# Kernel tuning notes

Measured on AMD Instinct MI355X. Metric: run time of the kernel, lower is better.

Reference implementation:

```python
import jax, jax.numpy as jnp
import numpy as np

N, E, D, ED = 10000, 50000, 32, 16
DIMS = [(D, 8 * D), (8 * D, 16 * D), (16 * D, 16 * D), (16 * D, 16 * D)]
BI_OUT = 8 * D + ED  # 272


def _gat(h, src, dst, ea, Wl, Wr, We, att, b, n):
    """GATv2Conv, heads=1: score = att . leaky_relu(Wl x_j + Wr x_i + We e_ij); msg = Wl x_j."""
    xl = h @ Wl
    xr = h @ Wr
    ee = ea @ We
    s = jax.nn.leaky_relu(xl[src] + xr[dst] + ee, 0.2)   # [E_aug, out]
    alpha = s @ att                                       # [E_aug]
    amax = jax.lax.stop_gradient(jax.ops.segment_max(alpha, dst, num_segments=n))
    ex = jnp.exp(alpha - amax[dst])
    den = jax.ops.segment_sum(ex, dst, num_segments=n)
    w = ex / jnp.maximum(den[dst], 1e-16)
    return jax.ops.segment_sum(xl[src] * w[:, None], dst, num_segments=n) + b


def _forward(x, edge_attr, Wl0, Wr0, We0, a0, b0, Wl1, Wr1, We1, a1, b1,
             Wl2, Wr2, We2, a2, b2, Wl3, Wr3, We3, a3, b3,
             Wbi, bbi, Wm1, bm1, Wm2, bm2, Wm3, bm3, edge_index):
    src, dst = edge_index[0], edge_index[1]
    # self loops with edge_attr fill_value='mean' (mean of incoming edge_attr per target node)
    cnt = jax.ops.segment_sum(jnp.ones((E,), jnp.float32), dst, num_segments=N)
    mean_attr = jax.ops.segment_sum(edge_attr, dst, num_segments=N) / jnp.maximum(cnt, 1.0)[:, None]
    loop = jnp.arange(N, dtype=edge_index.dtype)
    src_a = jnp.concatenate([src, loop])
    dst_a = jnp.concatenate([dst, loop])
    ea_a = jnp.concatenate([edge_attr, mean_attr], axis=0)

    h = x
    layers = [(Wl0, Wr0, We0, a0, b0), (Wl1, Wr1, We1, a1, b1),
              (Wl2, Wr2, We2, a2, b2), (Wl3, Wr3, We3, a3, b3)]
    for i, (Wl, Wr, We, a, b) in enumerate(layers):
        h = _gat(h, src_a, dst_a, ea_a, Wl, Wr, We, a, b, N)
        if i < 3:
            h = jax.nn.relu(h)

    # edge scoring: gather both endpoints, bilinear with edge_attr, then MLP -> sigmoid
    z = jnp.concatenate([h[src], h[dst]], axis=1)           # [E, 2*16*D] = [E, 1024]
    bi = jnp.einsum('ni,kij,nj->nk', z, Wbi, edge_attr) + bbi  # [E, 272]
    m = jax.nn.relu(bi @ Wm1 + bm1)
    m = jax.nn.relu(m @ Wm2 + bm2)
    return jax.nn.sigmoid(m @ Wm3 + bm3)                    # [E, 1]


def setup_inputs() -> dict:
    ki = iter(jax.random.split(jax.random.key(0), 40))

    def rn(shape, s=0.05):
        return jax.random.normal(next(ki), shape, dtype=jnp.float32) * s

    inp = {
        "x": rn((N, D), 1.0),
        "edge_attr": rn((E, ED), 1.0),
        "edge_index": jax.random.randint(next(ki), (2, E), 0, N, dtype=jnp.int32),
    }
    for i, (din, dout) in enumerate(DIMS):
        inp[f"Wl{i}"] = rn((din, dout))
        inp[f"Wr{i}"] = rn((din, dout))
        inp[f"We{i}"] = rn((ED, dout))
        inp[f"a{i}"] = rn((dout,))
        inp[f"b{i}"] = jnp.zeros((dout,), jnp.float32)
    inp["Wbi"] = rn((BI_OUT, 2 * 16 * D, ED), 0.02)
    inp["bbi"] = jnp.zeros((BI_OUT,), jnp.float32)
    inp["Wm1"] = rn((BI_OUT, BI_OUT))
    inp["bm1"] = jnp.zeros((BI_OUT,), jnp.float32)
    inp["Wm2"] = rn((BI_OUT, D))
    inp["bm2"] = jnp.zeros((D,), jnp.float32)
    inp["Wm3"] = rn((D, 1))
    inp["bm3"] = jnp.zeros((1,), jnp.float32)
    return inp


def reference(x, edge_attr, edge_index, Wl0, Wr0, We0, a0, b0, Wl1, Wr1, We1, a1, b1,
              Wl2, Wr2, We2, a2, b2, Wl3, Wr3, We3, a3, b3,
              Wbi, bbi, Wm1, bm1, Wm2, bm2, Wm3, bm3):
    return _forward(x, edge_attr, Wl0, Wr0, We0, a0, b0, Wl1, Wr1, We1, a1, b1,
                    Wl2, Wr2, We2, a2, b2, Wl3, Wr3, We3, a3, b3,
                    Wbi, bbi, Wm1, bm1, Wm2, bm2, Wm3, bm3, edge_index)
```

## Files before the change

### kernel.cpp

```cpp
#include <hip/hip_runtime.h>
#include <hip/hip_bf16.h>
#include <hip/hip_fp16.h>
#include <cstdio>

#define N_NODES 10000
#define M_NODEP 10240
#define N_EDGES 50000
#define M_EDGEP 50176
#define E_AUG   60000
#define E_AUGP  60160
#define ED      16
#define BI_OUT  272
#define KP      288

typedef __attribute__((ext_vector_type(8))) short s16x8;
typedef __attribute__((ext_vector_type(4))) short s16x4;
typedef __attribute__((ext_vector_type(8))) _Float16 h16x8;
typedef __attribute__((ext_vector_type(4))) _Float16 h16x4;
typedef __attribute__((ext_vector_type(4))) float f32x4;

__device__ inline void stc(float* p, float v){ *p = v; }
__device__ inline void stc(__hip_bfloat16* p, float v){ *p = __float2bfloat16(v); }
__device__ inline void stc(__half* p, float v){ *p = __float2half(v); }
__device__ inline float bf2f(short s){ return __uint_as_float(((unsigned)(unsigned short)s) << 16); }
__device__ inline short f2bf(float f){ __hip_bfloat16 h = __float2bfloat16(f); return *(short*)&h; }

__device__ __forceinline__ void gl2lds16(const void* g, void* l){
  __builtin_amdgcn_global_load_lds((const __attribute__((address_space(1))) void*)g,
                                   (__attribute__((address_space(3))) void*)l, 16, 0, 0);
}

__device__ inline size_t preidx(int n, int k, int kSteps){
  int nb = n >> 7, f = (n >> 4) & 7, r = n & 15;
  int s = k >> 5, q = (k >> 3) & 3, ii = k & 7;
  return ((((size_t)nb*kSteps + s)*8 + f)*64 + q*16 + r)*8 + ii;
}

__global__ void edge_attr_sum_k(const float* __restrict__ ea, const int* __restrict__ ei,
                                float* __restrict__ meanat, float* __restrict__ cntF){
  int t = blockIdx.x*256 + threadIdx.x;
  if (t >= N_EDGES*ED) return;
  int e = t >> 4, j = t & 15;
  int dst = ei[N_EDGES + e];
  atomicAdd(&meanat[dst*ED + j], ea[t]);
  if (j == 0) atomicAdd(&cntF[dst], 1.0f);
}

__global__ void mean_div_k(float* __restrict__ meanat, const float* __restrict__ cntF){
  int t = blockIdx.x*256 + threadIdx.x;
  if (t >= N_NODES*ED) return;
  meanat[t] /= fmaxf(cntF[t>>4], 1.0f);
}

__global__ void scan_k(const float* __restrict__ cntF, int* __restrict__ rowptr){
  __shared__ int s[1024];
  int tid = threadIdx.x;
  int loc[10]; int sum = 0;
  #pragma unroll
  for (int k = 0; k < 10; ++k){
    int i = tid*10 + k;
    int v = (i < N_NODES) ? ((int)cntF[i] + 1) : 0;
    loc[k] = sum; sum += v;
  }
  s[tid] = sum; __syncthreads();
  for (int off = 1; off < 1024; off <<= 1){
    int t2 = (tid >= off) ? s[tid-off] : 0;
    __syncthreads();
    s[tid] += t2;
    __syncthreads();
  }
  int pre = s[tid] - sum;
  #pragma unroll
  for (int k = 0; k < 10; ++k){
    int i = tid*10 + k;
    if (i < N_NODES) rowptr[i] = pre + loc[k];
  }
  if (tid == 1023) rowptr[N_NODES] = s[1023];
}

__global__ void scatter_k(const int* __restrict__ ei, const int* __restrict__ rowptr,
                          int* __restrict__ fill, int* __restrict__ csr){
  int e = blockIdx.x*256 + threadIdx.x;
  if (e >= E_AUG) return;
  int dst = (e < N_EDGES) ? ei[N_EDGES+e] : (e - N_EDGES);
  int pos = rowptr[dst] + atomicAdd(&fill[dst], 1);
  csr[pos] = e;
}

template<typename TC, bool BIAS, bool RELU>
__global__ __launch_bounds__(256)
void mfma_gemm_k(const __hip_bfloat16* __restrict__ A, const __hip_bfloat16* __restrict__ Bp,
                 TC* __restrict__ C, const float* __restrict__ bias,
                 int Mstore, int K, int lda, int ldc){
  __shared__ __align__(16) __hip_bfloat16 Asm[2][4096];
  const int tid = threadIdx.x;
  const int lane = tid & 63, wave = tid >> 6;
  const int wm = (wave >> 1) * 64, wn = (wave & 1) * 64;
  const int m0 = blockIdx.x * 128, n0 = blockIdx.y * 128;
  const int quad = lane >> 4, r16 = lane & 15;
  const int kSteps = K >> 5;

  f32x4 acc[4][4];
  #pragma unroll
  for (int i = 0; i < 4; ++i)
    #pragma unroll
    for (int j = 0; j < 4; ++j)
      acc[i][j] = (f32x4){0.f, 0.f, 0.f, 0.f};

  const int rl = lane >> 2, cq = lane & 3;
  const int row0 = wave*32 + rl;
  const int qg = (cq - ((row0 >> 1) & 3)) & 3;
  const __hip_bfloat16* ga0 = &A[(size_t)(m0 + row0)*lda + qg*8];
  const __hip_bfloat16* ga1 = &A[(size_t)(m0 + row0 + 16)*lda + qg*8];
  const int aoff0 = (wave*32)*32, aoff1 = (wave*32 + 16)*32;

  const __hip_bfloat16* gB = Bp + (((size_t)blockIdx.y*kSteps)*8 + (wn >> 4))*512 + (size_t)lane*8;

  gl2lds16(ga0, &Asm[0][aoff0]);
  gl2lds16(ga1, &Asm[0][aoff1]);
  s16x8 bcur[4], bnxt[4];
  #pragma unroll
  for (int j = 0; j < 4; ++j) bcur[j] = *(const s16x8*)(gB + j*512);

  for (int s = 0; s < kSteps; ++s){
    __syncthreads();
    if (s + 1 < kSteps){
      int k0 = (s + 1) * 32;
      gl2lds16(ga0 + k0, &Asm[(s+1)&1][aoff0]);
      gl2lds16(ga1 + k0, &Asm[(s+1)&1][aoff1]);
      const __hip_bfloat16* gBn = gB + (size_t)(s+1)*4096;
      #pragma unroll
      for (int j = 0; j < 4; ++j) bnxt[j] = *(const s16x8*)(gBn + j*512);
    }
    s16x8 af[4];
    #pragma unroll
    for (int i = 0; i < 4; ++i){
      int row = wm + i*16 + r16;
      af[i] = *(const s16x8*)&Asm[s & 1][row*32 + (((quad + (row >> 1)) & 3) << 3)];
    }
    #pragma unroll
    for (int i = 0; i < 4; ++i)
      #pragma unroll
      for (int j = 0; j < 4; ++j)
        acc[i][j] = __builtin_amdgcn_mfma_f32_16x16x32_bf16(af[i], bcur[j], acc[i][j], 0, 0, 0);
    #pragma unroll
    for (int j = 0; j < 4; ++j) bcur[j] = bnxt[j];
  }
  #pragma unroll
  for (int i = 0; i < 4; ++i){
    #pragma unroll
    for (int reg = 0; reg < 4; ++reg){
      int gr = m0 + wm + i*16 + quad*4 + reg;
      if (gr >= Mstore) continue;
      #pragma unroll
      for (int j = 0; j < 4; ++j){
        int gc = n0 + wn + j*16 + r16;
        float v = acc[i][j][reg];
        if (BIAS) v += bias[gc];
        if (RELU) v = fmaxf(v, 0.f);
        stc(&C[(size_t)gr*ldc + gc], v);
      }
    }
  }
}

__global__ void prep_weights_k(
    const float* __restrict__ Wl0, const float* __restrict__ Wr0, const float* __restrict__ We0,
    const float* __restrict__ Wl1, const float* __restrict__ Wr1, const float* __restrict__ We1,
    const float* __restrict__ Wl2, const float* __restrict__ Wr2, const float* __restrict__ We2,
    const float* __restrict__ Wl3, const float* __restrict__ Wr3, const float* __restrict__ We3,
    const float* __restrict__ Wm1, const float* __restrict__ bm1,
    const float* __restrict__ Wm2, const float* __restrict__ bm2,
    __hip_bfloat16* __restrict__ WTa, __hip_bfloat16* __restrict__ WeTa,
    __hip_bfloat16* __restrict__ Wm1T, __hip_bfloat16* __restrict__ Wm2T,
    float* __restrict__ bm1p, float* __restrict__ bm2p){
  int t = blockIdx.x*256 + threadIdx.x;
  if (t < 16384){
    int half = t >> 13, r = t & 8191, i = r >> 8, j = r & 255;
    WTa[preidx(half*256 + j, i, 1)] = __float2bfloat16(half ? Wr0[r] : Wl0[r]);
  } else if (t < 278528){
    int u = t - 16384, half = u >> 17, r = u & 131071, i = r >> 9, j = r & 511;
    WTa[16384 + preidx(half*512 + j, i, 8)] = __float2bfloat16(half ? Wr1[r] : Wl1[r]);
  } else if (t < 802816){
    int u = t - 278528, half = u >> 18, r = u & 262143, i = r >> 9, j = r & 511;
    WTa[278528 + preidx(half*512 + j, i, 16)] = __float2bfloat16(half ? Wr2[r] : Wl2[r]);
  } else if (t < 1327104){
    int u = t - 802816, half = u >> 18, r = u & 262143, i = r >> 9, j = r & 511;
    WTa[802816 + preidx(half*512 + j, i, 16)] = __float2bfloat16(half ? Wr3[r] : Wl3[r]);
  }
  if (t < 8192){
    int n = t >> 5, k = t & 31;
    WeTa[preidx(n, k, 1)] = __float2bfloat16((k < 16) ? We0[k*256 + n] : 0.f);
  } else if (t < 24576){
    int u = t - 8192, n = u >> 5, k = u & 31;
    WeTa[8192 + preidx(n, k, 1)] = __float2bfloat16((k < 16) ? We1[k*512 + n] : 0.f);
  } else if (t < 40960){
    int u = t - 24576, n = u >> 5, k = u & 31;
    WeTa[24576 + preidx(n, k, 1)] = __float2bfloat16((k < 16) ? We2[k*512 + n] : 0.f);
  } else if (t < 57344){
    int u = t - 40960, n = u >> 5, k = u & 31;
    WeTa[40960 + preidx(n, k, 1)] = __float2bfloat16((k < 16) ? We3[k*512 + n] : 0.f);
  }
  if (t < 384*KP){
    int n = t / KP, k = t - n*KP;
    Wm1T[preidx(n, k, 9)] = __float2bfloat16((n < BI_OUT && k < BI_OUT) ? Wm1[(size_t)k*BI_OUT + n] : 0.f);
  }
  if (t < 128*KP){
    int n = t / KP, k = t - n*KP;
    Wm2T[preidx(n, k, 9)] = __float2bfloat16((n < 32 && k < BI_OUT) ? Wm2[(size_t)k*32 + n] : 0.f);
  }
  if (t < 384) bm1p[t] = (t < BI_OUT) ? bm1[t] : 0.f;
  if (t < 128) bm2p[t] = (t < 32) ? bm2[t] : 0.f;
}

__global__ void cast_h_k(const float* __restrict__ h, __hip_bfloat16* __restrict__ hb, int K){
  int t = blockIdx.x*256 + threadIdx.x;
  if (t >= M_NODEP*K) return;
  int r = t / K;
  hb[t] = (r < N_NODES) ? __float2bfloat16(h[t]) : __float2bfloat16(0.f);
}

__global__ void cast_ea_k(const float* __restrict__ ea, const float* __restrict__ meanat,
                          __hip_bfloat16* __restrict__ eab){
  int t = blockIdx.x*256 + threadIdx.x;
  if (t >= E_AUGP*32) return;
  int e = t >> 5, j = t & 31;
  float v = 0.f;
  if (j < 16){
    if (e < N_EDGES) v = ea[(size_t)e*ED + j];
    else if (e < E_AUG) v = meanat[(size_t)(e - N_EDGES)*ED + j];
  }
  eab[t] = __float2bfloat16(v);
}

__global__ void wbi_transpose_k(const float* __restrict__ Wbi, __hip_bfloat16* __restrict__ WtAll){
  int t = blockIdx.x*256 + threadIdx.x;
  if (t >= BI_OUT*1024*ED) return;
  int k = t >> 14, r = t & 16383;
  int i = r >> 4, j = r & 15;
  int c = (k < 136) ? 0 : 1;
  int kb = c*136;
  const int cw = 2176;
  size_t baseE = (size_t)c * 2228224;
  int row = ((i >= 512) ? cw : 0) + (k - kb)*16 + j;
  WtAll[baseE + preidx(row, i & 511, 16)] = __float2bfloat16(Wbi[t]);
}

template<int DOUT, bool RELU>
__global__ __launch_bounds__(256)
void gat_fused_k(const __hip_bfloat16* __restrict__ XLXR, const __half* __restrict__ EE,
                 const int* __restrict__ ei, const int* __restrict__ rowptr,
                 const int* __restrict__ csr, const float* __restrict__ att,
                 const float* __restrict__ b, __hip_bfloat16* __restrict__ hb){
  constexpr int NI = DOUT/64;
  constexpr int W2 = 2*DOUT;
  int wave = threadIdx.x >> 6, lane = threadIdx.x & 63;
  int n = blockIdx.x*4 + wave;
  if (n >= N_NODES) return;
  int r0 = rowptr[n], r1 = rowptr[n+1];
  int pp = r0 + lane;
  int e_l = 0, s_l = 0;
  if (pp < r1){
    e_l = csr[pp];
    s_l = (e_l < N_EDGES) ? ei[e_l] : (e_l - N_EDGES);
  }
  float xr[NI], at[NI], acc[NI];
  #pragma unroll
  for (int i = 0; i < NI; ++i){
    int d = lane*NI + i;
    xr[i]  = bf2f(((const short*)XLXR)[(size_t)n*W2 + DOUT + d]);
    at[i]  = att[d];
    acc[i] = 0.f;
  }
  auto getes = [&](int p, int &e, int &s){
    int idx = p - r0;
    if (idx < 64){ e = __shfl(e_l, idx, 64); s = __shfl(s_l, idx, 64); }
    else { e = csr[p]; s = (e < N_EDGES) ? ei[e] : (e - N_EDGES); }
  };
  float mrun = -1e30f, den = 0.f;
  int p = r0;
  for (; p + 3 < r1; p += 4){
    int ee4[4], ss4[4];
    #pragma unroll
    for (int u = 0; u < 4; ++u) getes(p + u, ee4[u], ss4[u]);
    float xl[4][NI], a[4];
    #pragma unroll
    for (int u = 0; u < 4; ++u){
      const short* xp = (const short*)XLXR + (size_t)ss4[u]*W2 + lane*NI;
      const _Float16* ep = (const _Float16*)EE + (size_t)ee4[u]*DOUT + lane*NI;
      float au = 0.f;
      if constexpr (NI == 8){
        s16x8 xv = *(const s16x8*)xp; h16x8 ev = *(const h16x8*)ep;
        #pragma unroll
        for (int i = 0; i < 8; ++i){
          xl[u][i] = bf2f(xv[i]);
          float v = xl[u][i] + xr[i] + (float)ev[i];
          v = (v > 0.f) ? v : 0.2f*v;
          au += at[i]*v;
        }
      } else {
        s16x4 xv = *(const s16x4*)xp; h16x4 ev = *(const h16x4*)ep;
        #pragma unroll
        for (int i = 0; i < 4; ++i){
          xl[u][i] = bf2f(xv[i]);
          float v = xl[u][i] + xr[i] + (float)ev[i];
          v = (v > 0.f) ? v : 0.2f*v;
          au += at[i]*v;
        }
      }
      a[u] = au;
    }
    #pragma unroll
    for (int off = 32; off; off >>= 1){
      #pragma unroll
      for (int u = 0; u < 4; ++u) a[u] += __shfl_xor(a[u], off, 64);
    }
    float mnew = fmaxf(mrun, fmaxf(fmaxf(a[0], a[1]), fmaxf(a[2], a[3])));
    float sc = __expf(mrun - mnew);
    float w0 = __expf(a[0] - mnew), w1 = __expf(a[1] - mnew);
    float w2 = __expf(a[2] - mnew), w3 = __expf(a[3] - mnew);
    den = den*sc + w0 + w1 + w2 + w3;
    #pragma unroll
    for (int i = 0; i < NI; ++i)
      acc[i] = acc[i]*sc + w0*xl[0][i] + w1*xl[1][i] + w2*xl[2][i] + w3*xl[3][i];
    mrun = mnew;
  }
  for (; p + 1 < r1; p += 2){
    int e0, s0, e1, s1;
    getes(p, e0, s0); getes(p + 1, e1, s1);
    const short* xp0 = (const short*)XLXR + (size_t)s0*W2 + lane*NI;
    const short* xp1 = (const short*)XLXR + (size_t)s1*W2 + lane*NI;
    const _Float16* ep0 = (const _Float16*)EE + (size_t)e0*DOUT + lane*NI;
    const _Float16* ep1 = (const _Float16*)EE + (size_t)e1*DOUT + lane*NI;
    float xl0[NI], xl1[NI];
    float a0 = 0.f, a1 = 0.f;
    #pragma unroll
    for (int i = 0; i < NI; ++i){
      xl0[i] = bf2f(xp0[i]); xl1[i] = bf2f(xp1[i]);
      float v0 = xl0[i] + xr[i] + (float)ep0[i];
      float v1 = xl1[i] + xr[i] + (float)ep1[i];
      v0 = (v0 > 0.f) ? v0 : 0.2f*v0;
      v1 = (v1 > 0.f) ? v1 : 0.2f*v1;
      a0 += at[i]*v0; a1 += at[i]*v1;
    }
    #pragma unroll
    for (int off = 32; off; off >>= 1){
      a0 += __shfl_xor(a0, off, 64);
      a1 += __shfl_xor(a1, off, 64);
    }
    float mnew = fmaxf(mrun, fmaxf(a0, a1));
    float sc = __expf(mrun - mnew);
    float w0 = __expf(a0 - mnew);
    float w1 = __expf(a1 - mnew);
    den = den*sc + w0 + w1;
    #pragma unroll
    for (int i = 0; i < NI; ++i) acc[i] = acc[i]*sc + w0*xl0[i] + w1*xl1[i];
    mrun = mnew;
  }
  if (p < r1){
    int e0, s0;
    getes(p, e0, s0);
    const short* xp0 = (const short*)XLXR + (size_t)s0*W2 + lane*NI;
    const _Float16* ep0 = (const _Float16*)EE + (size_t)e0*DOUT + lane*NI;
    float xl0[NI];
    float a0 = 0.f;
    #pragma unroll
    for (int i = 0; i < NI; ++i){
      xl0[i] = bf2f(xp0[i]);
      float v0 = xl0[i] + xr[i] + (float)ep0[i];
      v0 = (v0 > 0.f) ? v0 : 0.2f*v0;
      a0 += at[i]*v0;
    }
    #pragma unroll
    for (int off = 32; off; off >>= 1) a0 += __shfl_xor(a0, off, 64);
    float mnew = fmaxf(mrun, a0);
    float sc = __expf(mrun - mnew);
    float w0 = __expf(a0 - mnew);
    den = den*sc + w0;
    #pragma unroll
    for (int i = 0; i < NI; ++i) acc[i] = acc[i]*sc + w0*xl0[i];
    mrun = mnew;
  }
  float dinv = 1.0f / fmaxf(den, 1e-16f);
  if constexpr (NI == 8){
    s16x8 o;
    #pragma unroll
    for (int i = 0; i < 8; ++i){
      float v = b[lane*8 + i] + acc[i]*dinv;
      o[i] = f2bf(RELU ? fmaxf(v, 0.f) : v);
    }
    *(s16x8*)((short*)hb + (size_t)n*DOUT + lane*8) = o;
  } else {
    s16x4 o;
    #pragma unroll
    for (int i = 0; i < 4; ++i){
      float v = b[lane*4 + i] + acc[i]*dinv;
      o[i] = f2bf(RELU ? fmaxf(v, 0.f) : v);
    }
    *(s16x4*)((short*)hb + (size_t)n*DOUT + lane*4) = o;
  }
}

__global__ void bi_k(const __hip_bfloat16* __restrict__ P, const float* __restrict__ ea,
                     const int* __restrict__ ei, const int* __restrict__ csr,
                     const float* __restrict__ bbi, __hip_bfloat16* __restrict__ bi,
                     int kb, int kcnt){
  int cw = kcnt*ED, w2 = 2*cw;
  int g = blockIdx.x*256 + threadIdx.x;
  if (g >= E_AUG*kcnt) return;
  int p = g / kcnt, k = g - p*kcnt;
  int e = csr[p];
  if (e >= N_EDGES) return;
  int src = ei[e], dst = ei[N_EDGES+e];
  const __hip_bfloat16* pl = P + (size_t)src*w2 + k*ED;
  const __hip_bfloat16* pr = P + (size_t)dst*w2 + cw + k*ED;
  const float* eap = ea + (size_t)e*ED;
  float s = 0.f;
  #pragma unroll
  for (int j = 0; j < ED; ++j)
    s += eap[j]*(__bfloat162float(pl[j]) + __bfloat162float(pr[j]));
  int kg = kb + k;
  bi[(size_t)e*KP + kg] = __float2bfloat16(s + bbi[kg]);
}

__global__ void out_k(const __hip_bfloat16* __restrict__ m2, const float* __restrict__ Wm3,
                      const float* __restrict__ bm3, float* __restrict__ out){
  int n = blockIdx.x*256 + threadIdx.x;
  if (n >= N_EDGES) return;
  float acc = bm3[0];
  #pragma unroll
  for (int j = 0; j < 32; ++j) acc += __bfloat162float(m2[(size_t)n*128 + j])*Wm3[j];
  out[n] = 1.0f/(1.0f + __expf(-acc));
}

extern "C" void kernel_launch(void* const* d_in, const int* in_sizes, int n_in,
                              void* d_out, int out_size, void* d_ws, size_t ws_size,
                              hipStream_t stream) {
  const float* x   = (const float*)d_in[0];
  const float* ea  = (const float*)d_in[1];
  const int*   ei  = (const int*)d_in[2];
  const float* Wl[4]  = {(const float*)d_in[3],(const float*)d_in[8],(const float*)d_in[13],(const float*)d_in[18]};
  const float* Wr[4]  = {(const float*)d_in[4],(const float*)d_in[9],(const float*)d_in[14],(const float*)d_in[19]};
  const float* We[4]  = {(const float*)d_in[5],(const float*)d_in[10],(const float*)d_in[15],(const float*)d_in[20]};
  const float* att[4] = {(const float*)d_in[6],(const float*)d_in[11],(const float*)d_in[16],(const float*)d_in[21]};
  const float* bia[4] = {(const float*)d_in[7],(const float*)d_in[12],(const float*)d_in[17],(const float*)d_in[22]};
  const float* Wbi = (const float*)d_in[23];
  const float* bbi = (const float*)d_in[24];
  const float* Wm1 = (const float*)d_in[25];
  const float* bm1 = (const float*)d_in[26];
  const float* Wm2 = (const float*)d_in[27];
  const float* bm2 = (const float*)d_in[28];
  const float* Wm3 = (const float*)d_in[29];
  const float* bm3 = (const float*)d_in[30];
  float* out = (float*)d_out;

  char* ws = (char*)d_ws;
  size_t off = 0;
  auto alloc = [&](size_t b){ off = (off + 255) & ~(size_t)255; size_t o = off; off += b; return o; };
  size_t o_bi   = alloc((size_t)M_EDGEP*KP*2);
  size_t o_XLXR = alloc((size_t)M_NODEP*1024*2);
  size_t o_hb   = alloc((size_t)M_NODEP*512*2);
  size_t o_eab  = alloc((size_t)E_AUGP*32*2);
  size_t o_WTa  = alloc((size_t)1327104*2);
  size_t o_WeTa = alloc((size_t)57344*2);
  size_t o_WtA  = alloc((size_t)8704*512*2);
  size_t o_EEP  = alloc((size_t)90000000);
  size_t o_Wm1T = alloc((size_t)384*KP*2);
  size_t o_Wm2T = alloc((size_t)128*KP*2);
  size_t o_bm1p = alloc(384*4);
  size_t o_bm2p = alloc(128*4);
  size_t o_ma   = alloc((size_t)N_NODES*ED*4);
  size_t o_cnt  = alloc(40000);
  size_t o_rp   = alloc(40004);
  size_t o_fill = alloc(40000);
  size_t o_csr  = alloc(240000);
  if (off > ws_size){
    fprintf(stderr, "kernel_launch: workspace too small: need %zu have %zu\n", off, ws_size);
    return;
  }

  float* meanat = (float*)(ws + o_ma);
  float* cntF   = (float*)(ws + o_cnt);
  int*   rowptr = (int*)(ws + o_rp);
  int*   fill   = (int*)(ws + o_fill);
  int*   csr    = (int*)(ws + o_csr);
  __hip_bfloat16* XLXR = (__hip_bfloat16*)(ws + o_XLXR);
  __hip_bfloat16* hb   = (__hip_bfloat16*)(ws + o_hb);
  __hip_bfloat16* eab  = (__hip_bfloat16*)(ws + o_eab);
  __hip_bfloat16* WTa  = (__hip_bfloat16*)(ws + o_WTa);
  __hip_bfloat16* WeTa = (__hip_bfloat16*)(ws + o_WeTa);
  __hip_bfloat16* WtA  = (__hip_bfloat16*)(ws + o_WtA);
  __half*        EE    = (__half*)(ws + o_EEP);
  __hip_bfloat16* P    = (__hip_bfloat16*)(ws + o_EEP);
  __hip_bfloat16* Wm1T = (__hip_bfloat16*)(ws + o_Wm1T);
  __hip_bfloat16* Wm2T = (__hip_bfloat16*)(ws + o_Wm2T);
  float* bm1p = (float*)(ws + o_bm1p);
  float* bm2p = (float*)(ws + o_bm2p);
  __hip_bfloat16* bi = (__hip_bfloat16*)(ws + o_bi);
  __hip_bfloat16* m1 = (__hip_bfloat16*)(ws + o_EEP);
  __hip_bfloat16* m2 = (__hip_bfloat16*)(ws + o_EEP + 40000000);

  hipMemsetAsync(ws + o_ma, 0, (o_cnt - o_ma) + 40000, stream);
  hipMemsetAsync(ws + o_fill, 0, 40000, stream);
  edge_attr_sum_k<<<3125, 256, 0, stream>>>(ea, ei, meanat, cntF);
  mean_div_k<<<625, 256, 0, stream>>>(meanat, cntF);
  scan_k<<<1, 1024, 0, stream>>>(cntF, rowptr);
  scatter_k<<<235, 256, 0, stream>>>(ei, rowptr, fill, csr);

  cast_h_k<<<(M_NODEP*32 + 255)/256, 256, 0, stream>>>(x, hb, 32);
  cast_ea_k<<<(E_AUGP*32 + 255)/256, 256, 0, stream>>>(ea, meanat, eab);
  prep_weights_k<<<5184, 256, 0, stream>>>(
      Wl[0], Wr[0], We[0], Wl[1], Wr[1], We[1], Wl[2], Wr[2], We[2], Wl[3], Wr[3], We[3],
      Wm1, bm1, Wm2, bm2, WTa, WeTa, Wm1T, Wm2T, bm1p, bm2p);
  wbi_transpose_k<<<(BI_OUT*1024*ED + 255)/256, 256, 0, stream>>>(Wbi, WtA);

  const int dins[4]  = {32, 256, 512, 512};
  const int douts[4] = {256, 512, 512, 512};
  const int wtOff[4] = {0, 16384, 278528, 802816};
  const int weOff[4] = {0, 8192, 24576, 40960};
  for (int L = 0; L < 4; ++L){
    int din = dins[L], dn = douts[L];
    dim3 g1(M_NODEP/128, 2*dn/128);
    mfma_gemm_k<__hip_bfloat16,false,false><<<g1, 256, 0, stream>>>(
        hb, WTa + wtOff[L], XLXR, nullptr, N_NODES, din, din, 2*dn);
    dim3 ge(E_AUGP/128, dn/128);
    mfma_gemm_k<__half,false,false><<<ge, 256, 0, stream>>>(
        eab, WeTa + weOff[L], EE, nullptr, E_AUG, 32, 32, dn);
    if (dn == 256)
      gat_fused_k<256,true><<<2500, 256, 0, stream>>>(XLXR, EE, ei, rowptr, csr, att[L], bia[L], hb);
    else if (L == 3)
      gat_fused_k<512,false><<<2500, 256, 0, stream>>>(XLXR, EE, ei, rowptr, csr, att[L], bia[L], hb);
    else
      gat_fused_k<512,true><<<2500, 256, 0, stream>>>(XLXR, EE, ei, rowptr, csr, att[L], bia[L], hb);
  }

  const int kbs[2]      = {0, 136};
  const int kcnts[2]    = {136, 136};
  const size_t baseE[2] = {0, 2228224};
  for (int c = 0; c < 2; ++c){
    int cw = kcnts[c]*ED, w2 = 2*cw;
    dim3 gp(M_NODEP/128, w2/128);
    mfma_gemm_k<__hip_bfloat16,false,false><<<gp, 256, 0, stream>>>(
        hb, WtA + baseE[c], P, nullptr, N_NODES, 512, 512, w2);
    bi_k<<<(E_AUG*kcnts[c] + 255)/256, 256, 0, stream>>>(P, ea, ei, csr, bbi, bi, kbs[c], kcnts[c]);
  }

  dim3 gm1(M_EDGEP/128, 3);
  mfma_gemm_k<__hip_bfloat16,true,true><<<gm1, 256, 0, stream>>>(bi, Wm1T, m1, bm1p, M_EDGEP, KP, KP, 384);
  dim3 gm2(M_EDGEP/128, 1);
  mfma_gemm_k<__hip_bfloat16,true,true><<<gm2, 256, 0, stream>>>(m1, Wm2T, m2, bm2p, M_EDGEP, KP, 384, 128);
  out_k<<<(N_EDGES + 255)/256, 256, 0, stream>>>(m2, Wm3, bm3, out);
}
```

Before: 632.2 us.

## Add K=32 multi-tile GEMM, fuse MLP2 with sigmoid output, vectorize bilinear

Adds a specialized GEMM for K=32 that loads the A tile once into shared memory and loops over all N tiles inside one block. It is used for the layer-0 node projection and the per-layer edge-attribute projection, so the A tile is not reloaded for each output column tile. The second MLP GEMM is fused with the final 32-wide dot product and sigmoid, computing only the 64 needed columns and skipping the m2 buffer and the separate out kernel. bi_k now computes two output features per thread using 16-byte vector loads, which hardcodes the chunk width of 136.

```diff
diff --git a/kernel.cpp b/kernel.cpp
--- a/kernel.cpp
+++ b/kernel.cpp
@@ -159,6 +159,148 @@
         if (BIAS) v += bias[gc];
         if (RELU) v = fmaxf(v, 0.f);
         stc(&C[(size_t)gr*ldc + gc], v);
+      }
+    }
+  }
+}
+
+template<typename TC>
+__global__ __launch_bounds__(256)
+void gemm_k32_k(const __hip_bfloat16* __restrict__ A, const __hip_bfloat16* __restrict__ Bp,
+                TC* __restrict__ C, int Mstore, int Ntiles, int lda, int ldc){
+  __shared__ __align__(16) __hip_bfloat16 Asm[4096];
+  const int tid = threadIdx.x;
+  const int lane = tid & 63, wave = tid >> 6;
+  const int wm = (wave >> 1) * 64, wn = (wave & 1) * 64;
+  const int m0 = blockIdx.x * 128;
+  const int quad = lane >> 4, r16 = lane & 15;
+
+  const int rl = lane >> 2, cq = lane & 3;
+  const int row0 = wave*32 + rl;
+  const int qg = (cq - ((row0 >> 1) & 3)) & 3;
+  gl2lds16(&A[(size_t)(m0 + row0)*lda + qg*8],      &Asm[(wave*32)*32]);
+  gl2lds16(&A[(size_t)(m0 + row0 + 16)*lda + qg*8], &Asm[(wave*32 + 16)*32]);
+  __syncthreads();
+  s16x8 af[4];
+  #pragma unroll
+  for (int i = 0; i < 4; ++i){
+    int row = wm + i*16 + r16;
+    af[i] = *(const s16x8*)&Asm[row*32 + (((quad + (row >> 1)) & 3) << 3)];
+  }
+
+  const __hip_bfloat16* gB = Bp + (size_t)(wn >> 4)*512 + (size_t)lane*8;
+  s16x8 bcur[4], bnxt[4];
+  #pragma unroll
+  for (int j = 0; j < 4; ++j) bcur[j] = *(const s16x8*)(gB + j*512);
+
+  for (int nt = 0; nt < Ntiles; ++nt){
+    if (nt + 1 < Ntiles){
+      const __hip_bfloat16* gBn = gB + (size_t)(nt+1)*4096;
+      #pragma unroll
+      for (int j = 0; j < 4; ++j) bnxt[j] = *(const s16x8*)(gBn + j*512);
+    }
+    f32x4 acc[4][4];
+    #pragma unroll
+    for (int i = 0; i < 4; ++i)
+      #pragma unroll
+      for (int j = 0; j < 4; ++j)
+        acc[i][j] = (f32x4){0.f, 0.f, 0.f, 0.f};
+    #pragma unroll
+    for (int i = 0; i < 4; ++i)
+      #pragma unroll
+      for (int j = 0; j < 4; ++j)
+        acc[i][j] = __builtin_amdgcn_mfma_f32_16x16x32_bf16(af[i], bcur[j], acc[i][j], 0, 0, 0);
+    int n0 = nt*128;
+    #pragma unroll
+    for (int i = 0; i < 4; ++i){
+      #pragma unroll
+      for (int reg = 0; reg < 4; ++reg){
+        int gr = m0 + wm + i*16 + quad*4 + reg;
+        if (gr >= Mstore) continue;
+        #pragma unroll
+        for (int j = 0; j < 4; ++j)
+          stc(&C[(size_t)gr*ldc + n0 + wn + j*16 + r16], acc[i][j][reg]);
+      }
+    }
+    #pragma unroll
+    for (int j = 0; j < 4; ++j) bcur[j] = bnxt[j];
+  }
+}
+
+__global__ __launch_bounds__(256)
+void mlp2_out_k(const __hip_bfloat16* __restrict__ A, const __hip_bfloat16* __restrict__ Bp,
+                const float* __restrict__ bias, const float* __restrict__ Wm3,
+                const float* __restrict__ bm3, float* __restrict__ out,
+                int Mstore, int K, int lda){
+  __shared__ __align__(16) __hip_bfloat16 Asm[2][4096];
+  const int tid = threadIdx.x;
+  const int lane = tid & 63, wave = tid >> 6;
+  const int wm = (wave >> 1) * 64, wn = (wave & 1) * 64;
+  const int m0 = blockIdx.x * 128;
+  const int quad = lane >> 4, r16 = lane & 15;
+  const int kSteps = K >> 5;
+
+  f32x4 acc[4][2];
+  #pragma unroll
+  for (int i = 0; i < 4; ++i)
+    #pragma unroll
+    for (int j = 0; j < 2; ++j)
+      acc[i][j] = (f32x4){0.f, 0.f, 0.f, 0.f};
+
+  const int rl = lane >> 2, cq = lane & 3;
+  const int row0 = wave*32 + rl;
+  const int qg = (cq - ((row0 >> 1) & 3)) & 3;
+  const __hip_bfloat16* ga0 = &A[(size_t)(m0 + row0)*lda + qg*8];
+  const __hip_bfloat16* ga1 = &A[(size_t)(m0 + row0 + 16)*lda + qg*8];
+  const int aoff0 = (wave*32)*32, aoff1 = (wave*32 + 16)*32;
+
+  const __hip_bfloat16* gB = Bp + (size_t)(wn >> 4)*512 + (size_t)lane*8;
+
+  gl2lds16(ga0, &Asm[0][aoff0]);
+  gl2lds16(ga1, &Asm[0][aoff1]);
+  s16x8 bcur[2], bnxt[2];
+  #pragma unroll
+  for (int j = 0; j < 2; ++j) bcur[j] = *(const s16x8*)(gB + j*512);
+
+  for (int s = 0; s < kSteps; ++s){
+    __syncthreads();
+    if (s + 1 < kSteps){
+      int k0 = (s + 1) * 32;
+      gl2lds16(ga0 + k0, &Asm[(s+1)&1][aoff0]);
+      gl2lds16(ga1 + k0, &Asm[(s+1)&1][aoff1]);
+      const __hip_bfloat16* gBn = gB + (size_t)(s+1)*4096;
+      #pragma unroll
+      for (int j = 0; j < 2; ++j) bnxt[j] = *(const s16x8*)(gBn + j*512);
+    }
+    s16x8 af[4];
+    #pragma unroll
+    for (int i = 0; i < 4; ++i){
+      int row = wm + i*16 + r16;
+      af[i] = *(const s16x8*)&Asm[s & 1][row*32 + (((quad + (row >> 1)) & 3) << 3)];
+    }
+    #pragma unroll
+    for (int i = 0; i < 4; ++i)
+      #pragma unroll
+      for (int j = 0; j < 2; ++j)
+        acc[i][j] = __builtin_amdgcn_mfma_f32_16x16x32_bf16(af[i], bcur[j], acc[i][j], 0, 0, 0);
+    #pragma unroll
+    for (int j = 0; j < 2; ++j) bcur[j] = bnxt[j];
+  }
+  if (wn == 0){
+    float w3a = Wm3[r16], w3b = Wm3[16 + r16];
+    float ba = bias[r16], bb = bias[16 + r16];
+    #pragma unroll
+    for (int i = 0; i < 4; ++i){
+      #pragma unroll
+      for (int reg = 0; reg < 4; ++reg){
+        int gr = m0 + wm + i*16 + quad*4 + reg;
+        float v0 = fmaxf(acc[i][0][reg] + ba, 0.f);
+        float v1 = fmaxf(acc[i][1][reg] + bb, 0.f);
+        float dot = v0*w3a + v1*w3b;
+        #pragma unroll
+        for (int off = 1; off < 16; off <<= 1) dot += __shfl_xor(dot, off, 64);
+        if (r16 == 0 && gr < Mstore)
+          out[gr] = 1.0f/(1.0f + __expf(-(dot + bm3[0])));
       }
     }
   }
@@ -404,33 +546,34 @@
 __global__ void bi_k(const __hip_bfloat16* __restrict__ P, const float* __restrict__ ea,
                      const int* __restrict__ ei, const int* __restrict__ csr,
                      const float* __restrict__ bbi, __hip_bfloat16* __restrict__ bi,
-                     int kb, int kcnt){
-  int cw = kcnt*ED, w2 = 2*cw;
+                     int kb){
+  const int KH = 68;
+  const int cw = 2176, w2 = 4352;
   int g = blockIdx.x*256 + threadIdx.x;
-  if (g >= E_AUG*kcnt) return;
-  int p = g / kcnt, k = g - p*kcnt;
+  if (g >= E_AUG*KH) return;
+  int p = g / KH, kp = g - p*KH;
+  int k = kp*2;
   int e = csr[p];
   if (e >= N_EDGES) return;
   int src = ei[e], dst = ei[N_EDGES+e];
-  const __hip_bfloat16* pl = P + (size_t)src*w2 + k*ED;
-  const __hip_bfloat16* pr = P + (size_t)dst*w2 + cw + k*ED;
+  const s16x8* pl = (const s16x8*)(P + (size_t)src*w2 + k*ED);
+  const s16x8* pr = (const s16x8*)(P + (size_t)dst*w2 + cw + k*ED);
+  s16x8 pl0 = pl[0], pl1 = pl[1], pl2 = pl[2], pl3 = pl[3];
+  s16x8 pr0 = pr[0], pr1 = pr[1], pr2 = pr[2], pr3 = pr[3];
   const float* eap = ea + (size_t)e*ED;
-  float s = 0.f;
-  #pragma unroll
-  for (int j = 0; j < ED; ++j)
-    s += eap[j]*(__bfloat162float(pl[j]) + __bfloat162float(pr[j]));
+  float s0 = 0.f, s1 = 0.f;
+  #pragma unroll
+  for (int j = 0; j < 8; ++j){
+    s0 += eap[j]  *(bf2f(pl0[j]) + bf2f(pr0[j]));
+    s0 += eap[j+8]*(bf2f(pl1[j]) + bf2f(pr1[j]));
+    s1 += eap[j]  *(bf2f(pl2[j]) + bf2f(pr2[j]));
+    s1 += eap[j+8]*(bf2f(pl3[j]) + bf2f(pr3[j]));
+  }
   int kg = kb + k;
-  bi[(size_t)e*KP + kg] = __float2bfloat16(s + bbi[kg]);
-}
-
-__global__ void out_k(const __hip_bfloat16* __restrict__ m2, const float* __restrict__ Wm3,
-                      const float* __restrict__ bm3, float* __restrict__ out){
-  int n = blockIdx.x*256 + threadIdx.x;
-  if (n >= N_EDGES) return;
-  float acc = bm3[0];
-  #pragma unroll
-  for (int j = 0; j < 32; ++j) acc += __bfloat162float(m2[(size_t)n*128 + j])*Wm3[j];
-  out[n] = 1.0f/(1.0f + __expf(-acc));
+  short2 o;
+  o.x = f2bf(s0 + bbi[kg]);
+  o.y = f2bf(s1 + bbi[kg+1]);
+  *(short2*)((short*)bi + (size_t)e*KP + kg) = o;
 }
 
 extern "C" void kernel_launch(void* const* d_in, const int* in_sizes, int n_in,
@@ -498,7 +641,6 @@
   float* bm2p = (float*)(ws + o_bm2p);
   __hip_bfloat16* bi = (__hip_bfloat16*)(ws + o_bi);
   __hip_bfloat16* m1 = (__hip_bfloat16*)(ws + o_EEP);
-  __hip_bfloat16* m2 = (__hip_bfloat16*)(ws + o_EEP + 40000000);
 
   hipMemsetAsync(ws + o_ma, 0, (o_cnt - o_ma) + 40000, stream);
   hipMemsetAsync(ws + o_fill, 0, 40000, stream);
@@ -520,12 +662,16 @@
   const int weOff[4] = {0, 8192, 24576, 40960};
   for (int L = 0; L < 4; ++L){
     int din = dins[L], dn = douts[L];
-    dim3 g1(M_NODEP/128, 2*dn/128);
-    mfma_gemm_k<__hip_bfloat16,false,false><<<g1, 256, 0, stream>>>(
-        hb, WTa + wtOff[L], XLXR, nullptr, N_NODES, din, din, 2*dn);
-    dim3 ge(E_AUGP/128, dn/128);
-    mfma_gemm_k<__half,false,false><<<ge, 256, 0, stream>>>(
-        eab, WeTa + weOff[L], EE, nullptr, E_AUG, 32, 32, dn);
+    if (L == 0){
+      gemm_k32_k<__hip_bfloat16><<<M_NODEP/128, 256, 0, stream>>>(
+          hb, WTa, XLXR, N_NODES, 4, 32, 512);
+    } else {
+      dim3 g1(M_NODEP/128, 2*dn/128);
+      mfma_gemm_k<__hip_bfloat16,false,false><<<g1, 256, 0, stream>>>(
+          hb, WTa + wtOff[L], XLXR, nullptr, N_NODES, din, din, 2*dn);
+    }
+    gemm_k32_k<__half><<<E_AUGP/128, 256, 0, stream>>>(
+        eab, WeTa + weOff[L], EE, E_AUG, dn/128, 32, dn);
     if (dn == 256)
       gat_fused_k<256,true><<<2500, 256, 0, stream>>>(XLXR, EE, ei, rowptr, csr, att[L], bia[L], hb);
     else if (L == 3)
@@ -535,19 +681,15 @@
   }
 
   const int kbs[2]      = {0, 136};
-  const int kcnts[2]    = {136, 136};
   const size_t baseE[2] = {0, 2228224};
   for (int c = 0; c < 2; ++c){
-    int cw = kcnts[c]*ED, w2 = 2*cw;
-    dim3 gp(M_NODEP/128, w2/128);
+    dim3 gp(M_NODEP/128, 4352/128);
     mfma_gemm_k<__hip_bfloat16,false,false><<<gp, 256, 0, stream>>>(
-        hb, WtA + baseE[c], P, nullptr, N_NODES, 512, 512, w2);
-    bi_k<<<(E_AUG*kcnts[c] + 255)/256, 256, 0, stream>>>(P, ea, ei, csr, bbi, bi, kbs[c], kcnts[c]);
+        hb, WtA + baseE[c], P, nullptr, N_NODES, 512, 512, 4352);
+    bi_k<<<(E_AUG*68 + 255)/256, 256, 0, stream>>>(P, ea, ei, csr, bbi, bi, kbs[c]);
   }
 
   dim3 gm1(M_EDGEP/128, 3);
   mfma_gemm_k<__hip_bfloat16,true,true><<<gm1, 256, 0, stream>>>(bi, Wm1T, m1, bm1p, M_EDGEP, KP, KP, 384);
-  dim3 gm2(M_EDGEP/128, 1);
-  mfma_gemm_k<__hip_bfloat16,true,true><<<gm2, 256, 0, stream>>>(m1, Wm2T, m2, bm2p, M_EDGEP, KP, 384, 128);
-  out_k<<<(N_EDGES + 255)/256, 256, 0, stream>>>(m2, Wm3, bm3, out);
-}
+  mlp2_out_k<<<M_EDGEP/128, 256, 0, stream>>>(m1, Wm2T, bm2p, Wm3, bm3, out, N_EDGES, KP, 384);
+}
```

Result: faster. 609.8 us (-3.5%).
